# Performance work log

Hardware: AMD Instinct MI355X
Metric: run time of the kernel (lower is better)

Reference implementation:

```python
import jax, jax.numpy as jnp
import numpy as np

BS, T, N = 16, 50, 100
OBS, ACT, HID, LAT = 40, 8, 64, 16
NEG = -9e15


def _gat(x, adj, w, a_src, a_dst, b, concat, alpha=0.2):
    # x: [B, n, fin]; w: [H, fin, fout]
    h = jnp.einsum('bni,hio->bhno', x, w)
    e_src = jnp.einsum('bhno,ho->bhn', h, a_src[..., 0])
    e_dst = jnp.einsum('bhno,ho->bhn', h, a_dst[..., 0])
    e = e_src[:, :, :, None] + e_dst[:, :, None, :]        # [B,H,n,n]
    e = jnp.where(e > 0, e, alpha * e)                     # LeakyReLU
    e = jnp.where(adj[None, None] > 0, e, NEG)             # mask by adjacency
    att = jax.nn.softmax(e, axis=-1)
    hp = jnp.einsum('bhnm,bhmo->bhno', att, h)
    if concat:
        B, H, n, fo = hp.shape
        return jax.nn.elu(hp.transpose(0, 2, 1, 3).reshape(B, n, H * fo) + b)
    return hp.mean(axis=1) + b


def _lstm(x, Wih, Whh, bih, bhh):
    # x: [B, T, H]; PyTorch gate order i, f, g, o
    def step(carry, xt):
        h, c = carry
        g = xt @ Wih + h @ Whh + bih + bhh
        i, f, gg, o = jnp.split(g, 4, axis=-1)
        c = jax.nn.sigmoid(f) * c + jax.nn.sigmoid(i) * jnp.tanh(gg)
        h = jax.nn.sigmoid(o) * jnp.tanh(c)
        return (h, c), h
    h0 = jnp.zeros((x.shape[0], Whh.shape[0]), x.dtype)
    _, ys = jax.lax.scan(step, (h0, h0), x.transpose(1, 0, 2))
    return ys.transpose(1, 0, 2)


def _forward(o, a_prev, m, eps, params, adj):
    (W_obs, b_obs, W_pa, b_pa, W_mk, b_mk, id_emb,
     lWih, lWhh, lbih, lbhh,
     e1w, e1s, e1d, e1b, e2w, e2s, e2d, e2b,
     d1w, d1s, d1d, d1b, d2w, d2s, d2d, d2b,
     d3w, d3s, d3d, d3b) = params
    bs, t, n, _ = o.shape
    # encode: summed embeddings (dropout is identity in eval)
    emb = (o @ W_obs + b_obs) + (a_prev @ W_pa + b_pa) + (m @ W_mk + b_mk) + id_emb[None, None]
    x = emb.transpose(0, 2, 1, 3).reshape(bs * n, t, HID)
    x = _lstm(x, lWih, lWhh, lbih, lbhh)
    x = x.reshape(bs, n, t, HID).transpose(0, 2, 1, 3).reshape(bs * t, n, HID)
    x = _gat(x, adj, e1w, e1s, e1d, e1b, True)
    x = _gat(x, adj, e2w, e2s, e2d, e2b, False)
    logits = x.reshape(bs, t, n, 2 * LAT).mean(axis=-2)    # AverageGlobalPool over nodes
    mu, logvar = jnp.split(logits, 2, axis=-1)
    z = mu + eps * jnp.exp(0.5 * logvar)                   # reparameterize
    zu = jnp.repeat(z[:, :, None, :], n, axis=2)           # RepeatGlobalUnpool
    d = jnp.concatenate([emb, zu], axis=-1).reshape(bs * t, n, HID + LAT)
    d = _gat(d, adj, d1w, d1s, d1d, d1b, True)
    d = _gat(d, adj, d2w, d2s, d2d, d2b, True)
    d = _gat(d, adj, d3w, d3s, d3d, d3b, False)
    a_recon = d.reshape(bs, t, n, ACT) * m
    return a_recon, mu, logvar


def setup_inputs() -> dict:
    key = jax.random.key(0)
    it = iter(jax.random.split(key, 48))
    def nrm(shape, s=0.1):
        return s * jax.random.normal(next(it), shape, jnp.float32)
    inp = {}
    inp['o'] = jax.random.normal(next(it), (BS, T, N, OBS), jnp.float32)
    inp['a_prev'] = jax.random.uniform(next(it), (BS, T, N, ACT), jnp.float32)
    inp['m'] = (jax.random.uniform(next(it), (BS, T, N, ACT)) > 0.5).astype(jnp.float32)
    inp['eps'] = jax.random.normal(next(it), (BS, T, LAT), jnp.float32)
    adj = jax.random.randint(next(it), (N, N), 0, 2).astype(jnp.int32)
    inp['adj'] = adj.at[jnp.arange(N), jnp.arange(N)].set(1)
    inp['W_obs'] = nrm((OBS, HID)); inp['b_obs'] = jnp.zeros((HID,), jnp.float32)
    inp['W_pa'] = nrm((ACT, HID)); inp['b_pa'] = jnp.zeros((HID,), jnp.float32)
    inp['W_mk'] = nrm((ACT, HID)); inp['b_mk'] = jnp.zeros((HID,), jnp.float32)
    inp['id_emb'] = nrm((N, HID), 1.0)
    inp['lWih'] = nrm((HID, 4 * HID)); inp['lWhh'] = nrm((HID, 4 * HID))
    inp['lbih'] = jnp.zeros((4 * HID,), jnp.float32); inp['lbhh'] = jnp.zeros((4 * HID,), jnp.float32)
    def gat_p(pfx, H, fin, fout, bdim):
        inp[pfx + 'w'] = nrm((H, fin, fout))
        inp[pfx + 's'] = nrm((H, fout, 1))
        inp[pfx + 'd'] = nrm((H, fout, 1))
        inp[pfx + 'b'] = jnp.zeros((bdim,), jnp.float32)
    gat_p('e1', 4, HID, HID // 4, HID)
    gat_p('e2', 1, HID, 2 * LAT, 2 * LAT)
    gat_p('d1', 4, LAT + HID, HID // 4, HID)
    gat_p('d2', 4, HID, HID // 4, HID)
    gat_p('d3', 1, HID, ACT, ACT)
    return inp


def reference(o, a_prev, m, eps, adj, W_obs, b_obs, W_pa, b_pa, W_mk, b_mk, id_emb,
              lWih, lWhh, lbih, lbhh,
              e1w, e1s, e1d, e1b, e2w, e2s, e2d, e2b,
              d1w, d1s, d1d, d1b, d2w, d2s, d2d, d2b,
              d3w, d3s, d3d, d3b):
    params = (W_obs, b_obs, W_pa, b_pa, W_mk, b_mk, id_emb,
              lWih, lWhh, lbih, lbhh,
              e1w, e1s, e1d, e1b, e2w, e2s, e2d, e2b,
              d1w, d1s, d1d, d1b, d2w, d2s, d2d, d2b,
              d3w, d3s, d3d, d3b)
    return _forward(o, a_prev, m, eps, params, adj)
```

## Files before the change

### kernel.cpp

```cpp
#include <hip/hip_runtime.h>

#define BS  16
#define TT  50
#define NN  100
#define OBSF 40
#define ACTF 8
#define HIDF 64
#define LATF 16

typedef __attribute__((ext_vector_type(8))) short bf16x8;
typedef __attribute__((ext_vector_type(4))) float f32x4;
typedef __fp16 f16x2 __attribute__((ext_vector_type(2)));

__device__ __forceinline__ float sigmf(float x) { return 1.f / (1.f + __expf(-x)); }
__device__ __forceinline__ float tanh_fast(float x) { return 1.f - 2.f / (__expf(2.f * x) + 1.f); }
__device__ __forceinline__ short bf16s_rne(float a) {
    unsigned u = __float_as_uint(a); u += 0x7fffu + ((u >> 16) & 1u);
    return (short)(u >> 16);
}
__device__ __forceinline__ unsigned bf16pk_rne(float a, float b) {
    unsigned ua = __float_as_uint(a); ua += 0x7fffu + ((ua >> 16) & 1u);
    unsigned ub = __float_as_uint(b); ub += 0x7fffu + ((ub >> 16) & 1u);
    return (ua >> 16) | (ub & 0xffff0000u);
}

__global__ void adjmask_kernel(const int* __restrict__ adj, unsigned long long* __restrict__ mask) {
    int n = threadIdx.x;
    if (n < NN) {
        unsigned long long w0 = 0ull, w1 = 0ull;
        for (int m = 0; m < 64; ++m)  if (adj[n * NN + m] > 0) w0 |= (1ull << m);
        for (int m = 64; m < NN; ++m) if (adj[n * NN + m] > 0) w1 |= (1ull << (m - 64));
        mask[2 * n] = w0; mask[2 * n + 1] = w1;
    }
}

__global__ void emb_kernel(const float* __restrict__ o, const float* __restrict__ ap,
                           const float* __restrict__ mk,
                           const float* __restrict__ Wobs, const float* __restrict__ bobs,
                           const float* __restrict__ Wpa, const float* __restrict__ bpa,
                           const float* __restrict__ Wmk, const float* __restrict__ bmk,
                           const float* __restrict__ idemb, float* __restrict__ emb) {
    int g = blockIdx.x;
    int n = g % NN;
    int j = threadIdx.x;
    __shared__ float so[OBSF], sa[ACTF], sm[ACTF];
    if (j < OBSF) so[j] = o[(size_t)g * OBSF + j];
    if (j >= 40 && j < 48) sa[j - 40] = ap[(size_t)g * ACTF + (j - 40)];
    if (j >= 48 && j < 56) sm[j - 48] = mk[(size_t)g * ACTF + (j - 48)];
    __syncthreads();
    float acc = bobs[j] + bpa[j] + bmk[j] + idemb[n * HIDF + j];
    #pragma unroll
    for (int k = 0; k < OBSF; ++k) acc += so[k] * Wobs[k * HIDF + j];
    #pragma unroll
    for (int k = 0; k < ACTF; ++k) acc += sa[k] * Wpa[k * HIDF + j] + sm[k] * Wmk[k * HIDF + j];
    emb[(size_t)g * HIDF + j] = acc;
}

__launch_bounds__(256)
__global__ void lstm_mfma_kernel(const float* __restrict__ emb,
                                 const float* __restrict__ Wih, const float* __restrict__ Whh,
                                 const float* __restrict__ bih, const float* __restrict__ bhh,
                                 float* __restrict__ xenc) {
    constexpr int GSTRIDE = 260;
    __shared__ __align__(16) float gbuf[16 * GSTRIDE];
    __shared__ __align__(16) short embt[2][16 * 72];
    __shared__ __align__(16) short hbuf[16 * 72];

    const int tid = threadIdx.x;
    const int wv = tid >> 6, lane = tid & 63, q = lane >> 4, c = lane & 15;

    const int seq = tid >> 4;
    const int part = tid & 15;
    const int s = blockIdx.x * 16 + seq;
    const int b = s / NN, n = s % NN;
    const size_t ebase = ((size_t)b * (TT * NN) + n) * HIDF + part * 4;
    const int u0 = part * 4;
    const size_t xbase = ((size_t)b * (TT * NN) + n) * HIDF + u0;

    union { short s8[8]; bf16x8 v; } bf[2][2][4];
    {
        const int colb = wv * 64 + c;
        #pragma unroll
        for (int m = 0; m < 2; ++m) {
            const float* W = m ? Whh : Wih;
            #pragma unroll
            for (int kc = 0; kc < 2; ++kc)
                #pragma unroll
                for (int nt = 0; nt < 4; ++nt)
                    #pragma unroll
                    for (int j = 0; j < 8; ++j)
                        bf[m][kc][nt].s8[j] = bf16s_rne(W[(size_t)(kc * 32 + q * 8 + j) * 256 + colb + nt * 16]);
        }
    }
    float4 bi, bfo, bg, bo;
    {
        float* bp[4] = {&bi.x, &bfo.x, &bg.x, &bo.x};
        #pragma unroll
        for (int gsel = 0; gsel < 4; ++gsel)
            #pragma unroll
            for (int r = 0; r < 4; ++r)
                bp[gsel][r] = bih[gsel * 64 + u0 + r] + bhh[gsel * 64 + u0 + r];
    }
    for (int i = tid; i < 16 * 72 / 2; i += 256) ((unsigned*)hbuf)[i] = 0u;
    {
        float4 e0 = *(const float4*)&emb[ebase];
        uint2 pk; pk.x = bf16pk_rne(e0.x, e0.y); pk.y = bf16pk_rne(e0.z, e0.w);
        *(uint2*)&embt[0][seq * 72 + part * 4] = pk;
    }
    float cst[4] = {0.f, 0.f, 0.f, 0.f};
    __syncthreads();

    for (int t = 0; t < TT; ++t) {
        float4 pre;
        if (t + 1 < TT) pre = *(const float4*)&emb[ebase + (size_t)(t + 1) * (NN * HIDF)];
        const short* et = &embt[t & 1][0];
        bf16x8 a_e0 = *(const bf16x8*)&et[c * 72 + q * 8];
        bf16x8 a_e1 = *(const bf16x8*)&et[c * 72 + 32 + q * 8];
        bf16x8 a_h0 = *(const bf16x8*)&hbuf[c * 72 + q * 8];
        bf16x8 a_h1 = *(const bf16x8*)&hbuf[c * 72 + 32 + q * 8];
        f32x4 acc[4];
        #pragma unroll
        for (int nt = 0; nt < 4; ++nt) {
            f32x4 a = {0.f, 0.f, 0.f, 0.f};
            a = __builtin_amdgcn_mfma_f32_16x16x32_bf16(a_e0, bf[0][0][nt].v, a, 0, 0, 0);
            a = __builtin_amdgcn_mfma_f32_16x16x32_bf16(a_e1, bf[0][1][nt].v, a, 0, 0, 0);
            a = __builtin_amdgcn_mfma_f32_16x16x32_bf16(a_h0, bf[1][0][nt].v, a, 0, 0, 0);
            a = __builtin_amdgcn_mfma_f32_16x16x32_bf16(a_h1, bf[1][1][nt].v, a, 0, 0, 0);
            acc[nt] = a;
        }
        #pragma unroll
        for (int nt = 0; nt < 4; ++nt)
            #pragma unroll
            for (int r = 0; r < 4; ++r)
                gbuf[(q * 4 + r) * GSTRIDE + wv * 64 + nt * 16 + c] = acc[nt][r];
        __syncthreads();
        if (t + 1 < TT) {
            uint2 pk; pk.x = bf16pk_rne(pre.x, pre.y); pk.y = bf16pk_rne(pre.z, pre.w);
            *(uint2*)&embt[(t + 1) & 1][seq * 72 + part * 4] = pk;
        }
        float4 gi = *(const float4*)&gbuf[seq * GSTRIDE + u0];
        float4 gf = *(const float4*)&gbuf[seq * GSTRIDE + 64 + u0];
        float4 gg = *(const float4*)&gbuf[seq * GSTRIDE + 128 + u0];
        float4 go = *(const float4*)&gbuf[seq * GSTRIDE + 192 + u0];
        float hv[4];
        {
            float gir[4] = {gi.x + bi.x, gi.y + bi.y, gi.z + bi.z, gi.w + bi.w};
            float gfr[4] = {gf.x + bfo.x, gf.y + bfo.y, gf.z + bfo.z, gf.w + bfo.w};
            float ggr[4] = {gg.x + bg.x, gg.y + bg.y, gg.z + bg.z, gg.w + bg.w};
            float gor[4] = {go.x + bo.x, go.y + bo.y, go.z + bo.z, go.w + bo.w};
            #pragma unroll
            for (int r = 0; r < 4; ++r) {
                cst[r] = sigmf(gfr[r]) * cst[r] + sigmf(gir[r]) * tanh_fast(ggr[r]);
                hv[r] = sigmf(gor[r]) * tanh_fast(cst[r]);
            }
        }
        uint2 hpk; hpk.x = bf16pk_rne(hv[0], hv[1]); hpk.y = bf16pk_rne(hv[2], hv[3]);
        *(uint2*)&hbuf[seq * 72 + u0] = hpk;
        float4 xo; xo.x = hv[0]; xo.y = hv[1]; xo.z = hv[2]; xo.w = hv[3];
        *(float4*)&xenc[xbase + (size_t)t * (NN * HIDF)] = xo;
        __syncthreads();
    }
}

template <int FIN2>
__launch_bounds__(256)
__global__ void gat4h_kernel(const float* __restrict__ x1, const float* __restrict__ x2,
                             const float* __restrict__ w, const float* __restrict__ asrc,
                             const float* __restrict__ adst, const float* __restrict__ bias,
                             const unsigned long long* __restrict__ adjmask,
                             float* __restrict__ out) {
    constexpr int FIN = 64 + FIN2;
    __shared__ __align__(16) char regA[112 * 72 * 2];
    __shared__ __align__(16) short swb[64 * 72];
    __shared__ __align__(16) short wab[16 * 72];
    __shared__ __align__(16) float ses[4 * 112];
    __shared__ __align__(16) float sed[4 * 112];
    __shared__ float szd[64];
    __shared__ float sesc[4], sedc[4];
    __shared__ unsigned long long smask[2 * NN];
    short* sxa = (short*)regA;
    __fp16* sh16 = (__fp16*)regA;

    const int g = blockIdx.x, tid = threadIdx.x;
    const int wv = tid >> 6, lane = tid & 63, q = lane >> 4, c = lane & 15;

    for (int i = tid; i < 112 * 36; i += 256) {
        int n = i / 36, k2 = i % 36, k = 2 * k2;
        float lo = 0.f, hi = 0.f;
        if (n < NN && k < 64) {
            float2 v = *(const float2*)&x1[((size_t)g * NN + n) * 64 + k];
            lo = v.x; hi = v.y;
        }
        ((unsigned*)sxa)[i] = bf16pk_rne(lo, hi);
    }
    for (int i = tid; i < 64 * 36; i += 256) {
        int nc = i / 36, k2 = i % 36, k = 2 * k2;
        int h = nc >> 4, o = nc & 15;
        float lo = 0.f, hi = 0.f;
        if (k < 64) {
            lo = w[((size_t)h * FIN + k) * 16 + o];
            hi = w[((size_t)h * FIN + k + 1) * 16 + o];
        }
        ((unsigned*)swb)[i] = bf16pk_rne(lo, hi);
    }
    for (int i = tid; i < 16 * 36; i += 256) {
        int col = i / 36, k2 = i % 36, k = 2 * k2;
        float lo = 0.f, hi = 0.f;
        if (col < 8 && k < 64) {
            int h = col >> 1;
            const float* av = (col & 1) ? adst : asrc;
            float s0 = 0.f, s1 = 0.f;
            #pragma unroll
            for (int o = 0; o < 16; ++o) {
                float a = av[h * 16 + o];
                s0 += w[((size_t)h * FIN + k) * 16 + o] * a;
                s1 += w[((size_t)h * FIN + k + 1) * 16 + o] * a;
            }
            lo = s0; hi = s1;
        }
        ((unsigned*)wab)[i] = bf16pk_rne(lo, hi);
    }
    if constexpr (FIN2 > 0) {
        if (tid < 64) {
            int h = tid >> 4, o = tid & 15;
            float s = 0.f;
            #pragma unroll
            for (int k = 0; k < FIN2; ++k)
                s += x2[(size_t)g * FIN2 + k] * w[((size_t)h * FIN + 64 + k) * 16 + o];
            szd[tid] = s;
        }
    }
    if (tid < 2 * NN) smask[tid] = adjmask[tid];
    __syncthreads();

    if constexpr (FIN2 > 0) {
        if (tid < 8) {
            int h = tid >> 1;
            const float* av = (tid & 1) ? adst : asrc;
            float s = 0.f;
            #pragma unroll
            for (int o = 0; o < 16; ++o) s += szd[h * 16 + o] * av[h * 16 + o];
            if (tid & 1) sedc[h] = s; else sesc[h] = s;
        }
    }

    f32x4 hc[7], ec[7];
    #pragma unroll
    for (int mt = 0; mt < 7; ++mt) {
        hc[mt] = f32x4{0.f, 0.f, 0.f, 0.f};
        ec[mt] = f32x4{0.f, 0.f, 0.f, 0.f};
    }
    #pragma unroll
    for (int kc = 0; kc < 2; ++kc) {
        bf16x8 bfr = *(const bf16x8*)&swb[(wv * 16 + c) * 72 + kc * 32 + q * 8];
        bf16x8 wfr = *(const bf16x8*)&wab[c * 72 + kc * 32 + q * 8];
        #pragma unroll
        for (int mt = 0; mt < 7; ++mt) {
            bf16x8 afr = *(const bf16x8*)&sxa[(mt * 16 + c) * 72 + kc * 32 + q * 8];
            hc[mt] = __builtin_amdgcn_mfma_f32_16x16x32_bf16(afr, bfr, hc[mt], 0, 0, 0);
            ec[mt] = __builtin_amdgcn_mfma_f32_16x16x32_bf16(afr, wfr, ec[mt], 0, 0, 0);
        }
    }
    float zdv = 0.f, escv = 0.f, edcv = 0.f;
    if constexpr (FIN2 > 0) {
        zdv = szd[wv * 16 + c];
        escv = sesc[wv]; edcv = sedc[wv];
    }
    __syncthreads();

    #pragma unroll
    for (int mt = 0; mt < 7; ++mt) {
        f16x2 p01, p23;
        p01[0] = (__fp16)(hc[mt][0] + zdv); p01[1] = (__fp16)(hc[mt][1] + zdv);
        p23[0] = (__fp16)(hc[mt][2] + zdv); p23[1] = (__fp16)(hc[mt][3] + zdv);
        f16x2* dst = (f16x2*)&sh16[(wv * 16 + c) * 120 + mt * 16 + q * 4];
        dst[0] = p01; dst[1] = p23;
        int nb = wv * 112 + mt * 16 + q * 4;
        if (c == 2 * wv) {
            ses[nb + 0] = ec[mt][0] + escv; ses[nb + 1] = ec[mt][1] + escv;
            ses[nb + 2] = ec[mt][2] + escv; ses[nb + 3] = ec[mt][3] + escv;
        } else if (c == 2 * wv + 1) {
            sed[nb + 0] = ec[mt][0] + edcv; sed[nb + 1] = ec[mt][1] + edcv;
            sed[nb + 2] = ec[mt][2] + edcv; sed[nb + 3] = ec[mt][3] + edcv;
        }
    }
    __syncthreads();

    for (int idx = tid; idx < 4 * NN; idx += 256) {
        int h2 = idx / NN;
        int n = idx % NN;
        unsigned long long m0 = smask[2 * n], m1 = smask[2 * n + 1];
        float esn = ses[h2 * 112 + n];
        float denom = 0.f;
        float acc[16];
        #pragma unroll
        for (int qq = 0; qq < 16; ++qq) acc[qq] = 0.f;
        const float4* sedf4 = (const float4*)&sed[h2 * 112];
        const __fp16* hb = &sh16[(h2 * 16) * 120];
        #pragma unroll 2
        for (int gg = 0; gg < 13; ++gg) {
            unsigned mb = (gg < 8) ? (unsigned)(m0 >> (8 * gg)) & 0xffu
                                   : (unsigned)(m1 >> (8 * (gg - 8))) & 0xffu;
            float4 edA = sedf4[2 * gg];
            float4 edB = sedf4[2 * gg + 1];
            float e0 = esn + edA.x; e0 = fmaxf(e0, 0.2f * e0);
            float e1 = esn + edA.y; e1 = fmaxf(e1, 0.2f * e1);
            float e2 = esn + edA.z; e2 = fmaxf(e2, 0.2f * e2);
            float e3 = esn + edA.w; e3 = fmaxf(e3, 0.2f * e3);
            float e4 = esn + edB.x; e4 = fmaxf(e4, 0.2f * e4);
            float e5 = esn + edB.y; e5 = fmaxf(e5, 0.2f * e5);
            float e6 = esn + edB.z; e6 = fmaxf(e6, 0.2f * e6);
            float e7 = esn + edB.w; e7 = fmaxf(e7, 0.2f * e7);
            float p0 = (mb & 1u)   ? __expf(e0) : 0.f;
            float p1 = (mb & 2u)   ? __expf(e1) : 0.f;
            float p2 = (mb & 4u)   ? __expf(e2) : 0.f;
            float p3 = (mb & 8u)   ? __expf(e3) : 0.f;
            float p4 = (mb & 16u)  ? __expf(e4) : 0.f;
            float p5 = (mb & 32u)  ? __expf(e5) : 0.f;
            float p6 = (mb & 64u)  ? __expf(e6) : 0.f;
            float p7 = (mb & 128u) ? __expf(e7) : 0.f;
            denom += ((p0 + p1) + (p2 + p3)) + ((p4 + p5) + (p6 + p7));
            f16x2 q01 = __builtin_amdgcn_cvt_pkrtz(p0, p1);
            f16x2 q23 = __builtin_amdgcn_cvt_pkrtz(p2, p3);
            f16x2 q45 = __builtin_amdgcn_cvt_pkrtz(p4, p5);
            f16x2 q67 = __builtin_amdgcn_cvt_pkrtz(p6, p7);
            #pragma unroll
            for (int oo = 0; oo < 16; ++oo) {
                const f16x2* hp = (const f16x2*)&hb[oo * 120 + gg * 8];
                float a = acc[oo];
                a = __builtin_amdgcn_fdot2(q01, hp[0], a, false);
                a = __builtin_amdgcn_fdot2(q23, hp[1], a, false);
                a = __builtin_amdgcn_fdot2(q45, hp[2], a, false);
                a = __builtin_amdgcn_fdot2(q67, hp[3], a, false);
                acc[oo] = a;
            }
        }
        float inv = 1.f / denom;
        float4* op = (float4*)&out[((size_t)g * NN + n) * 64 + h2 * 16];
        #pragma unroll
        for (int q4 = 0; q4 < 4; ++q4) {
            float4 v;
            float a0 = acc[4 * q4 + 0] * inv + bias[h2 * 16 + 4 * q4 + 0];
            float a1 = acc[4 * q4 + 1] * inv + bias[h2 * 16 + 4 * q4 + 1];
            float a2 = acc[4 * q4 + 2] * inv + bias[h2 * 16 + 4 * q4 + 2];
            float a3 = acc[4 * q4 + 3] * inv + bias[h2 * 16 + 4 * q4 + 3];
            v.x = (a0 > 0.f) ? a0 : (__expf(a0) - 1.f);
            v.y = (a1 > 0.f) ? a1 : (__expf(a1) - 1.f);
            v.z = (a2 > 0.f) ? a2 : (__expf(a2) - 1.f);
            v.w = (a3 > 0.f) ? a3 : (__expf(a3) - 1.f);
            op[q4] = v;
        }
    }
}

template <int FIN1, int FIN2, int H, int FOUT, int SPLIT, int OUTMODE>
__launch_bounds__(256)
__global__ void gat_kernel(const float* __restrict__ x1, const float* __restrict__ x2,
                           const float* __restrict__ w, const float* __restrict__ asrc,
                           const float* __restrict__ adst, const float* __restrict__ bias,
                           const unsigned long long* __restrict__ adjmask,
                           const float* __restrict__ mgate, float* __restrict__ out) {
    constexpr int FIN = FIN1 + FIN2;
    constexpr int HF = H * FOUT;
    constexpr int NPT = 256 / HF;
    constexpr int ROWS = (NN + NPT - 1) / NPT;
    constexpr int SXB = NN * FIN1 * 4;
    constexpr int SHB = HF * 120 * 2;
    constexpr int R1 = (SXB > SHB) ? SXB : SHB;
    __shared__ __align__(16) char smem[R1];
    float* sx = (float*)smem;
    __fp16* sh16 = (__fp16*)smem;
    __shared__ float sz[FIN2 > 0 ? FIN2 : 1];
    __shared__ __align__(16) float ses[H * 112];
    __shared__ __align__(16) float sed[H * 112];
    __shared__ unsigned long long smask[2 * NN];
    int g = blockIdx.x;
    int tid = threadIdx.x;

    for (int i = tid; i < NN * FIN1; i += 256) {
        int n = i / FIN1, k = i % FIN1;
        sx[n * FIN1 + k] = x1[((size_t)g * NN + n) * FIN1 + k];
    }
    if constexpr (FIN2 > 0) {
        if (tid < FIN2) sz[tid] = x2[(size_t)g * FIN2 + tid];
    }
    if (tid < 2 * NN) smask[tid] = adjmask[tid];
    __syncthreads();

    const int ho = tid % HF;
    const int h = ho / FOUT, o = ho % FOUT;
    const int n0 = tid / HF;
    float racc[ROWS];
    {
        float wcol[FIN];
        #pragma unroll
        for (int k = 0; k < FIN; ++k) wcol[k] = w[((size_t)h * FIN + k) * FOUT + o];
        float zdot = 0.f;
        if constexpr (FIN2 > 0) {
            #pragma unroll
            for (int k = 0; k < FIN2; ++k) zdot += sz[k] * wcol[FIN1 + k];
        }
        const float as = asrc[ho], ad = adst[ho];
        #pragma unroll
        for (int r = 0; r < ROWS; ++r) {
            int n = n0 + r * NPT;
            float acc = zdot;
            if (ROWS * NPT == NN || n < NN) {
                const float4* row = (const float4*)&sx[n * FIN1];
                #pragma unroll
                for (int k4 = 0; k4 < FIN1 / 4; ++k4) {
                    float4 xv = row[k4];
                    acc += xv.x * wcol[4 * k4] + xv.y * wcol[4 * k4 + 1]
                         + xv.z * wcol[4 * k4 + 2] + xv.w * wcol[4 * k4 + 3];
                }
            }
            racc[r] = acc;
            float vs = acc * as, vd = acc * ad;
            #pragma unroll
            for (int off = FOUT / 2; off >= 1; off >>= 1) {
                vs += __shfl_xor(vs, off, 64);
                vd += __shfl_xor(vd, off, 64);
            }
            if (o == 0 && (ROWS * NPT == NN || n < NN)) {
                ses[h * 112 + n] = vs; sed[h * 112 + n] = vd;
            }
        }
    }
    __syncthreads();
    #pragma unroll
    for (int r = 0; r < ROWS; ++r) {
        int n = n0 + r * NPT;
        if (ROWS * NPT == NN || n < NN) sh16[ho * 120 + n] = (__fp16)racc[r];
    }
    for (int i = tid; i < HF * 20; i += 256)
        sh16[(i / 20) * 120 + 100 + (i % 20)] = (__fp16)0.f;
    for (int i = tid; i < H * 12; i += 256)
        sed[(i / 12) * 112 + 100 + (i % 12)] = 0.f;
    __syncthreads();

    constexpr int FT = FOUT / SPLIT;
    constexpr int ITEMS = H * NN * SPLIT;
    for (int idx = tid; idx < ITEMS; idx += 256) {
        int h2 = idx / (NN * SPLIT);
        int rem = idx % (NN * SPLIT);
        int n = rem / SPLIT;
        int os = (rem % SPLIT) * FT;
        unsigned long long m0 = smask[2 * n], m1 = smask[2 * n + 1];
        float esn = ses[h2 * 112 + n];
        float denom = 0.f;
        float acc[FT];
        #pragma unroll
        for (int qq = 0; qq < FT; ++qq) acc[qq] = 0.f;
        const float4* sedf4 = (const float4*)&sed[h2 * 112];
        const __fp16* hb = &sh16[(h2 * FOUT + os) * 120];
        #pragma unroll 2
        for (int gg = 0; gg < 13; ++gg) {
            unsigned mb = (gg < 8) ? (unsigned)(m0 >> (8 * gg)) & 0xffu
                                   : (unsigned)(m1 >> (8 * (gg - 8))) & 0xffu;
            float4 edA = sedf4[2 * gg];
            float4 edB = sedf4[2 * gg + 1];
            float e0 = esn + edA.x; e0 = fmaxf(e0, 0.2f * e0);
            float e1 = esn + edA.y; e1 = fmaxf(e1, 0.2f * e1);
            float e2 = esn + edA.z; e2 = fmaxf(e2, 0.2f * e2);
            float e3 = esn + edA.w; e3 = fmaxf(e3, 0.2f * e3);
            float e4 = esn + edB.x; e4 = fmaxf(e4, 0.2f * e4);
            float e5 = esn + edB.y; e5 = fmaxf(e5, 0.2f * e5);
            float e6 = esn + edB.z; e6 = fmaxf(e6, 0.2f * e6);
            float e7 = esn + edB.w; e7 = fmaxf(e7, 0.2f * e7);
            float p0 = (mb & 1u)   ? __expf(e0) : 0.f;
            float p1 = (mb & 2u)   ? __expf(e1) : 0.f;
            float p2 = (mb & 4u)   ? __expf(e2) : 0.f;
            float p3 = (mb & 8u)   ? __expf(e3) : 0.f;
            float p4 = (mb & 16u)  ? __expf(e4) : 0.f;
            float p5 = (mb & 32u)  ? __expf(e5) : 0.f;
            float p6 = (mb & 64u)  ? __expf(e6) : 0.f;
            float p7 = (mb & 128u) ? __expf(e7) : 0.f;
            denom += ((p0 + p1) + (p2 + p3)) + ((p4 + p5) + (p6 + p7));
            f16x2 q01 = __builtin_amdgcn_cvt_pkrtz(p0, p1);
            f16x2 q23 = __builtin_amdgcn_cvt_pkrtz(p2, p3);
            f16x2 q45 = __builtin_amdgcn_cvt_pkrtz(p4, p5);
            f16x2 q67 = __builtin_amdgcn_cvt_pkrtz(p6, p7);
            #pragma unroll
            for (int oo = 0; oo < FT; ++oo) {
                const f16x2* hp = (const f16x2*)&hb[oo * 120 + gg * 8];
                float a = acc[oo];
                a = __builtin_amdgcn_fdot2(q01, hp[0], a, false);
                a = __builtin_amdgcn_fdot2(q23, hp[1], a, false);
                a = __builtin_amdgcn_fdot2(q45, hp[2], a, false);
                a = __builtin_amdgcn_fdot2(q67, hp[3], a, false);
                acc[oo] = a;
            }
        }
        float inv = 1.f / denom;
        if constexpr (OUTMODE == 1) {
            float4* op = (float4*)&out[((size_t)g * NN + n) * FOUT + os];
            #pragma unroll
            for (int q4 = 0; q4 < FT / 4; ++q4) {
                float4 v;
                v.x = acc[4 * q4 + 0] * inv + bias[os + 4 * q4 + 0];
                v.y = acc[4 * q4 + 1] * inv + bias[os + 4 * q4 + 1];
                v.z = acc[4 * q4 + 2] * inv + bias[os + 4 * q4 + 2];
                v.w = acc[4 * q4 + 3] * inv + bias[os + 4 * q4 + 3];
                op[q4] = v;
            }
        } else {
            size_t base = ((size_t)g * NN + n) * FOUT + os;
            float4* op = (float4*)&out[base];
            const float4* mp = (const float4*)&mgate[base];
            #pragma unroll
            for (int q4 = 0; q4 < FT / 4; ++q4) {
                float4 mv = mp[q4];
                float4 v;
                v.x = (acc[4 * q4 + 0] * inv + bias[os + 4 * q4 + 0]) * mv.x;
                v.y = (acc[4 * q4 + 1] * inv + bias[os + 4 * q4 + 1]) * mv.y;
                v.z = (acc[4 * q4 + 2] * inv + bias[os + 4 * q4 + 2]) * mv.z;
                v.w = (acc[4 * q4 + 3] * inv + bias[os + 4 * q4 + 3]) * mv.w;
                op[q4] = v;
            }
        }
    }
}

__global__ void pool_kernel(const float* __restrict__ g2, const float* __restrict__ eps,
                            float* __restrict__ z, float* __restrict__ dout) {
    int g = blockIdx.x;
    int c = threadIdx.x;
    __shared__ float s[2 * LATF];
    if (c < 2 * LATF) {
        float sum = 0.f;
        for (int n = 0; n < NN; ++n) sum += g2[((size_t)g * NN + n) * (2 * LATF) + c];
        s[c] = sum * (1.f / NN);
    }
    __syncthreads();
    if (c < LATF) {
        float mu = s[c], lv = s[LATF + c];
        dout[640000 + (size_t)g * LATF + c] = mu;
        dout[652800 + (size_t)g * LATF + c] = lv;
        z[(size_t)g * LATF + c] = mu + eps[(size_t)g * LATF + c] * __expf(0.5f * lv);
    }
}

extern "C" void kernel_launch(void* const* d_in, const int* in_sizes, int n_in,
                              void* d_out, int out_size, void* d_ws, size_t ws_size,
                              hipStream_t stream) {
    const float* o     = (const float*)d_in[0];
    const float* aprev = (const float*)d_in[1];
    const float* mk    = (const float*)d_in[2];
    const float* eps   = (const float*)d_in[3];
    const int*   adj   = (const int*)d_in[4];
    const float* Wobs  = (const float*)d_in[5];
    const float* bobs  = (const float*)d_in[6];
    const float* Wpa   = (const float*)d_in[7];
    const float* bpa   = (const float*)d_in[8];
    const float* Wmk   = (const float*)d_in[9];
    const float* bmk   = (const float*)d_in[10];
    const float* idemb = (const float*)d_in[11];
    const float* lWih  = (const float*)d_in[12];
    const float* lWhh  = (const float*)d_in[13];
    const float* lbih  = (const float*)d_in[14];
    const float* lbhh  = (const float*)d_in[15];
    const float* e1w = (const float*)d_in[16]; const float* e1s = (const float*)d_in[17];
    const float* e1d = (const float*)d_in[18]; const float* e1b = (const float*)d_in[19];
    const float* e2w = (const float*)d_in[20]; const float* e2s = (const float*)d_in[21];
    const float* e2d = (const float*)d_in[22]; const float* e2b = (const float*)d_in[23];
    const float* d1w = (const float*)d_in[24]; const float* d1s = (const float*)d_in[25];
    const float* d1d = (const float*)d_in[26]; const float* d1b = (const float*)d_in[27];
    const float* d2w = (const float*)d_in[28]; const float* d2s = (const float*)d_in[29];
    const float* d2d = (const float*)d_in[30]; const float* d2b = (const float*)d_in[31];
    const float* d3w = (const float*)d_in[32]; const float* d3s = (const float*)d_in[33];
    const float* d3d = (const float*)d_in[34]; const float* d3b = (const float*)d_in[35];

    float* ws   = (float*)d_ws;
    float* emb  = ws;
    float* xenc = ws + 5120000;
    float* g1o  = ws + 10240000;
    float* g2o  = ws + 15360000;
    float* z    = ws + 17920000;
    float* d1o  = ws + 18000000;
    float* d2o  = ws + 23200000;
    unsigned long long* amask = (unsigned long long*)(ws + 30720000);
    float* out = (float*)d_out;

    adjmask_kernel<<<1, 128, 0, stream>>>(adj, amask);
    emb_kernel<<<BS * TT * NN, 64, 0, stream>>>(o, aprev, mk, Wobs, bobs, Wpa, bpa,
                                                Wmk, bmk, idemb, emb);
    lstm_mfma_kernel<<<100, 256, 0, stream>>>(emb, lWih, lWhh, lbih, lbhh, xenc);
    gat4h_kernel<0><<<800, 256, 0, stream>>>(xenc, nullptr, e1w, e1s, e1d, e1b, amask, g1o);
    gat_kernel<64, 0, 1, 32, 4, 1><<<800, 256, 0, stream>>>(g1o, nullptr, e2w, e2s, e2d, e2b,
                                                            amask, nullptr, g2o);
    pool_kernel<<<800, 64, 0, stream>>>(g2o, eps, z, out);
    gat4h_kernel<16><<<800, 256, 0, stream>>>(emb, z, d1w, d1s, d1d, d1b, amask, d1o);
    gat4h_kernel<0><<<800, 256, 0, stream>>>(d1o, nullptr, d2w, d2s, d2d, d2b, amask, d2o);
    gat_kernel<64, 0, 1, 8, 2, 2><<<800, 256, 0, stream>>>(d2o, nullptr, d3w, d3s, d3d, d3b,
                                                           amask, mk, out);
}
```

Before: 480.5 us.

## Remap LSTM weight columns so each wave owns all four gates per unit

The LSTM weight fragments are reordered so each wave's four MFMA output tiles cover the i, f, g and o gates of the same 16 hidden units. The gate nonlinearity can then run directly on the accumulator registers, with no round trip through a shared gate buffer. The hidden state is double-buffered in LDS, which removes one of the two barriers per timestep. In exchange, the xenc output stores become scalar and strided rather than float4, and the hidden-state LDS writes become per-element shorts.

```diff
diff --git a/kernel.cpp b/kernel.cpp
--- a/kernel.cpp
+++ b/kernel.cpp
@@ -61,47 +61,47 @@
                                  const float* __restrict__ Wih, const float* __restrict__ Whh,
                                  const float* __restrict__ bih, const float* __restrict__ bhh,
                                  float* __restrict__ xenc) {
-    constexpr int GSTRIDE = 260;
-    __shared__ __align__(16) float gbuf[16 * GSTRIDE];
     __shared__ __align__(16) short embt[2][16 * 72];
-    __shared__ __align__(16) short hbuf[16 * 72];
+    __shared__ __align__(16) short hbuf[2][16 * 72];
 
     const int tid = threadIdx.x;
     const int wv = tid >> 6, lane = tid & 63, q = lane >> 4, c = lane & 15;
 
     const int seq = tid >> 4;
     const int part = tid & 15;
-    const int s = blockIdx.x * 16 + seq;
-    const int b = s / NN, n = s % NN;
-    const size_t ebase = ((size_t)b * (TT * NN) + n) * HIDF + part * 4;
-    const int u0 = part * 4;
-    const size_t xbase = ((size_t)b * (TT * NN) + n) * HIDF + u0;
+    const int s_st = blockIdx.x * 16 + seq;
+    const int b_st = s_st / NN, n_st = s_st % NN;
+    const size_t ebase = ((size_t)b_st * (TT * NN) + n_st) * HIDF + part * 4;
+
+    const int unit = wv * 16 + c;
 
     union { short s8[8]; bf16x8 v; } bf[2][2][4];
-    {
-        const int colb = wv * 64 + c;
-        #pragma unroll
-        for (int m = 0; m < 2; ++m) {
-            const float* W = m ? Whh : Wih;
-            #pragma unroll
-            for (int kc = 0; kc < 2; ++kc)
+    #pragma unroll
+    for (int m = 0; m < 2; ++m) {
+        const float* W = m ? Whh : Wih;
+        #pragma unroll
+        for (int kc = 0; kc < 2; ++kc)
+            #pragma unroll
+            for (int gsel = 0; gsel < 4; ++gsel)
                 #pragma unroll
-                for (int nt = 0; nt < 4; ++nt)
-                    #pragma unroll
-                    for (int j = 0; j < 8; ++j)
-                        bf[m][kc][nt].s8[j] = bf16s_rne(W[(size_t)(kc * 32 + q * 8 + j) * 256 + colb + nt * 16]);
-        }
-    }
-    float4 bi, bfo, bg, bo;
-    {
-        float* bp[4] = {&bi.x, &bfo.x, &bg.x, &bo.x};
-        #pragma unroll
-        for (int gsel = 0; gsel < 4; ++gsel)
-            #pragma unroll
-            for (int r = 0; r < 4; ++r)
-                bp[gsel][r] = bih[gsel * 64 + u0 + r] + bhh[gsel * 64 + u0 + r];
-    }
-    for (int i = tid; i < 16 * 72 / 2; i += 256) ((unsigned*)hbuf)[i] = 0u;
+                for (int j = 0; j < 8; ++j)
+                    bf[m][kc][gsel].s8[j] =
+                        bf16s_rne(W[(size_t)(kc * 32 + q * 8 + j) * 256 + gsel * 64 + unit]);
+    }
+    const float bgi = bih[unit] + bhh[unit];
+    const float bgf = bih[64 + unit] + bhh[64 + unit];
+    const float bgg = bih[128 + unit] + bhh[128 + unit];
+    const float bgo = bih[192 + unit] + bhh[192 + unit];
+
+    size_t xb[4];
+    #pragma unroll
+    for (int r = 0; r < 4; ++r) {
+        int s = blockIdx.x * 16 + q * 4 + r;
+        int b = s / NN, n = s % NN;
+        xb[r] = ((size_t)b * (TT * NN) + n) * HIDF + unit;
+    }
+
+    for (int i = tid; i < 16 * 72 / 2; i += 256) ((unsigned*)hbuf[0])[i] = 0u;
     {
         float4 e0 = *(const float4*)&emb[ebase];
         uint2 pk; pk.x = bf16pk_rne(e0.x, e0.y); pk.y = bf16pk_rne(e0.z, e0.w);
@@ -113,51 +113,42 @@
     for (int t = 0; t < TT; ++t) {
         float4 pre;
         if (t + 1 < TT) pre = *(const float4*)&emb[ebase + (size_t)(t + 1) * (NN * HIDF)];
-        const short* et = &embt[t & 1][0];
+        const short* et = embt[t & 1];
+        const short* hb = hbuf[t & 1];
         bf16x8 a_e0 = *(const bf16x8*)&et[c * 72 + q * 8];
         bf16x8 a_e1 = *(const bf16x8*)&et[c * 72 + 32 + q * 8];
-        bf16x8 a_h0 = *(const bf16x8*)&hbuf[c * 72 + q * 8];
-        bf16x8 a_h1 = *(const bf16x8*)&hbuf[c * 72 + 32 + q * 8];
+        bf16x8 a_h0 = *(const bf16x8*)&hb[c * 72 + q * 8];
+        bf16x8 a_h1 = *(const bf16x8*)&hb[c * 72 + 32 + q * 8];
         f32x4 acc[4];
         #pragma unroll
-        for (int nt = 0; nt < 4; ++nt) {
+        for (int gsel = 0; gsel < 4; ++gsel) {
             f32x4 a = {0.f, 0.f, 0.f, 0.f};
-            a = __builtin_amdgcn_mfma_f32_16x16x32_bf16(a_e0, bf[0][0][nt].v, a, 0, 0, 0);
-            a = __builtin_amdgcn_mfma_f32_16x16x32_bf16(a_e1, bf[0][1][nt].v, a, 0, 0, 0);
-            a = __builtin_amdgcn_mfma_f32_16x16x32_bf16(a_h0, bf[1][0][nt].v, a, 0, 0, 0);
-            a = __builtin_amdgcn_mfma_f32_16x16x32_bf16(a_h1, bf[1][1][nt].v, a, 0, 0, 0);
-            acc[nt] = a;
-        }
-        #pragma unroll
-        for (int nt = 0; nt < 4; ++nt)
-            #pragma unroll
-            for (int r = 0; r < 4; ++r)
-                gbuf[(q * 4 + r) * GSTRIDE + wv * 64 + nt * 16 + c] = acc[nt][r];
-        __syncthreads();
+            a = __builtin_amdgcn_mfma_f32_16x16x32_bf16(a_e0, bf[0][0][gsel].v, a, 0, 0, 0);
+            a = __builtin_amdgcn_mfma_f32_16x16x32_bf16(a_e1, bf[0][1][gsel].v, a, 0, 0, 0);
+            a = __builtin_amdgcn_mfma_f32_16x16x32_bf16(a_h0, bf[1][0][gsel].v, a, 0, 0, 0);
+            a = __builtin_amdgcn_mfma_f32_16x16x32_bf16(a_h1, bf[1][1][gsel].v, a, 0, 0, 0);
+            acc[gsel] = a;
+        }
+        float hv[4];
+        #pragma unroll
+        for (int r = 0; r < 4; ++r) {
+            float gi = acc[0][r] + bgi;
+            float gf = acc[1][r] + bgf;
+            float gg = acc[2][r] + bgg;
+            float go = acc[3][r] + bgo;
+            cst[r] = sigmf(gf) * cst[r] + sigmf(gi) * tanh_fast(gg);
+            hv[r] = sigmf(go) * tanh_fast(cst[r]);
+        }
+        short* hn = hbuf[(t + 1) & 1];
+        #pragma unroll
+        for (int r = 0; r < 4; ++r) {
+            hn[(q * 4 + r) * 72 + unit] = bf16s_rne(hv[r]);
+            xenc[xb[r] + (size_t)t * (NN * HIDF)] = hv[r];
+        }
         if (t + 1 < TT) {
             uint2 pk; pk.x = bf16pk_rne(pre.x, pre.y); pk.y = bf16pk_rne(pre.z, pre.w);
             *(uint2*)&embt[(t + 1) & 1][seq * 72 + part * 4] = pk;
         }
-        float4 gi = *(const float4*)&gbuf[seq * GSTRIDE + u0];
-        float4 gf = *(const float4*)&gbuf[seq * GSTRIDE + 64 + u0];
-        float4 gg = *(const float4*)&gbuf[seq * GSTRIDE + 128 + u0];
-        float4 go = *(const float4*)&gbuf[seq * GSTRIDE + 192 + u0];
-        float hv[4];
-        {
-            float gir[4] = {gi.x + bi.x, gi.y + bi.y, gi.z + bi.z, gi.w + bi.w};
-            float gfr[4] = {gf.x + bfo.x, gf.y + bfo.y, gf.z + bfo.z, gf.w + bfo.w};
-            float ggr[4] = {gg.x + bg.x, gg.y + bg.y, gg.z + bg.z, gg.w + bg.w};
-            float gor[4] = {go.x + bo.x, go.y + bo.y, go.z + bo.z, go.w + bo.w};
-            #pragma unroll
-            for (int r = 0; r < 4; ++r) {
-                cst[r] = sigmf(gfr[r]) * cst[r] + sigmf(gir[r]) * tanh_fast(ggr[r]);
-                hv[r] = sigmf(gor[r]) * tanh_fast(cst[r]);
-            }
-        }
-        uint2 hpk; hpk.x = bf16pk_rne(hv[0], hv[1]); hpk.y = bf16pk_rne(hv[2], hv[3]);
-        *(uint2*)&hbuf[seq * 72 + u0] = hpk;
-        float4 xo; xo.x = hv[0]; xo.y = hv[1]; xo.z = hv[2]; xo.w = hv[3];
-        *(float4*)&xenc[xbase + (size_t)t * (NN * HIDF)] = xo;
         __syncthreads();
     }
 }
```

Measured after the change: 488.8 us. About the same (+1.7%).
